# Performance work log

Measured on AMD Instinct MI355X. Metric: run time of the kernel, lower is better.

## Reference

```python
import jax, jax.numpy as jnp
import numpy as np

BETA = 0.25
N_CODES = 1024
CODE_DIM = 64


def setup_inputs() -> dict:
    key = jax.random.key(0)
    k1, k2 = jax.random.split(key)
    z_e = jax.random.normal(k1, (32, CODE_DIM, 2048), dtype=jnp.float32)
    # nn.init.uniform_(weight, -1/n_codes, 1/n_codes)
    lim = 1.0 / N_CODES
    codebook = jax.random.uniform(k2, (N_CODES, CODE_DIM), dtype=jnp.float32,
                                  minval=-lim, maxval=lim)
    return {"z_e": z_e, "codebook": codebook}


def reference(z_e, codebook):
    B, C, K = z_e.shape
    # (B, C, K) -> (B*K, C)
    z = jnp.transpose(z_e, (0, 2, 1)).reshape(-1, C)
    # squared L2 distances: ||z||^2 + ||e||^2 - 2 z.e  -> (N, n_codes)
    dist = (jnp.sum(z * z, axis=1, keepdims=True)
            + jnp.sum(codebook * codebook, axis=1)[None, :]
            - 2.0 * (z @ codebook.T))
    codes = jnp.argmin(dist, axis=1)  # (N,)
    # gather quantized vectors, back to (B, C, K)
    z_q = jnp.transpose(codebook[codes].reshape(B, K, C), (0, 2, 1))
    # straight-through
    z_q_st = z_e + jax.lax.stop_gradient(z_q - z_e)
    sg = jax.lax.stop_gradient
    loss_codebook = jnp.mean((z_q - sg(z_e)) ** 2)
    loss_commit = jnp.mean((z_e - sg(z_q)) ** 2)
    loss_vq = loss_codebook + BETA * loss_commit
    # perplexity via histogram (equivalent to onehot.mean(0))
    n = codes.shape[0]
    avg_probs = jnp.zeros((N_CODES,), dtype=jnp.float32).at[codes].add(1.0) / n
    perplexity = jnp.exp(-jnp.sum(avg_probs * jnp.log(avg_probs + 1e-10)))
    return z_q_st, codes.reshape(B, K), loss_vq, perplexity
```

## Files before the change

### kernel.cpp

```cpp
#include <hip/hip_runtime.h>
#include <math.h>

#define NB 32
#define NC 64
#define NK 2048
#define NCODES 1024
#define NVEC (NB*NK)
#define NELEM (NB*NC*NK)
#define NBLK (NVEC/64)

#define MARGIN 1.5e-3f
#define CAP 32

#define WS_HIST  0
#define WS_CBN32 4096
#define WS_PART  8192
#define WS_CTR   16384
#define WS_CBBF  32768

typedef __bf16 bf16x8 __attribute__((ext_vector_type(8)));
typedef float  f32x4  __attribute__((ext_vector_type(4)));
#define MFMA16(A, B, ACC) __builtin_amdgcn_mfma_f32_16x16x32_bf16(A, B, ACC, 0, 0, 0)

__global__ void k_cbprep(const float* __restrict__ cb, float* __restrict__ n32,
                         __bf16* __restrict__ cbbf, int* __restrict__ hist,
                         unsigned int* __restrict__ ctr) {
    const int t = threadIdx.x;
    const int j = blockIdx.x * 64 + t;
    if (blockIdx.x == 0) {
        int4 z4; z4.x = 0; z4.y = 0; z4.z = 0; z4.w = 0;
#pragma unroll
        for (int i = 0; i < 4; i++) ((int4*)hist)[t * 4 + i] = z4;
        if (t == 0) *ctr = 0u;
    }
    const float* cr = cb + (size_t)j * NC;
    float x[64];
#pragma unroll
    for (int i = 0; i < 16; i++) {
        f32x4 tv = *(const f32x4*)(cr + 4 * i);
        x[4*i+0] = tv[0]; x[4*i+1] = tv[1]; x[4*i+2] = tv[2]; x[4*i+3] = tv[3];
    }
    float r[8];
#pragma unroll
    for (int q = 0; q < 8; q++) r[q] = __fmul_rn(x[q], x[q]);
#pragma unroll
    for (int i = 8; i < 64; i += 8)
#pragma unroll
        for (int q = 0; q < 8; q++)
            r[q] = __fadd_rn(r[q], __fmul_rn(x[i + q], x[i + q]));
    float s01 = __fadd_rn(r[0], r[1]), s23 = __fadd_rn(r[2], r[3]);
    float s45 = __fadd_rn(r[4], r[5]), s67 = __fadd_rn(r[6], r[7]);
    n32[j] = __fadd_rn(__fadd_rn(s01, s23), __fadd_rn(s45, s67));
    __bf16* br = cbbf + (size_t)j * NC;
#pragma unroll
    for (int i = 0; i < 8; i++) {
        bf16x8 o;
#pragma unroll
        for (int q = 0; q < 8; q++) o[q] = (__bf16)x[8*i + q];
        *(bf16x8*)(br + 8*i) = o;
    }
}

__launch_bounds__(256, 4)
__global__ void k_vq(const float* __restrict__ ze, const float* __restrict__ cb,
                     const float* __restrict__ n32, const __bf16* __restrict__ cbbf,
                     int* __restrict__ hist, float* __restrict__ codes_f,
                     float* __restrict__ outq, double* __restrict__ part,
                     unsigned int* __restrict__ ctr, float* __restrict__ outsc) {
    __shared__ float zl[64 * 65];
    __shared__ float nl[NCODES];
    __shared__ float wmin[64][4];
    __shared__ float gthr[64];
    __shared__ int cnt[64];
    __shared__ int cand[64][CAP];
    __shared__ unsigned long long keys2[64][4];
    __shared__ int codearr[64];
    __shared__ double lsd[4];
    __shared__ int lastflag;
    __shared__ double TL[16], TE[16];

    const int t = threadIdx.x;
    const int L = t & 63;
    const int w = t >> 6;
    const int quad = L >> 4;
    const int col = L & 15;
    const int vec0 = blockIdx.x * 64;
    const int b = vec0 >> 11;
    const int k0 = vec0 & (NK - 1);
    const float* zbase = ze + (size_t)b * NC * NK + k0;

#pragma unroll
    for (int i = 0; i < 4; i++) {
        int idx = t + i * 256;
        int c = idx >> 4, vq = (idx & 15) * 4;
        f32x4 val = *(const f32x4*)(zbase + (size_t)c * NK + vq);
        zl[c * 65 + vq + 0] = val[0];
        zl[c * 65 + vq + 1] = val[1];
        zl[c * 65 + vq + 2] = val[2];
        zl[c * 65 + vq + 3] = val[3];
        nl[idx] = n32[idx];
    }
    __syncthreads();

    bf16x8 af[4][2];
#pragma unroll
    for (int vt = 0; vt < 4; vt++)
#pragma unroll
        for (int kt = 0; kt < 2; kt++)
#pragma unroll
            for (int j = 0; j < 8; j++)
                af[vt][kt][j] =
                    (__bf16)zl[(kt*32 + quad*8 + j) * 65 + vt*16 + col];

    float pmin[4][4];
#pragma unroll
    for (int vt = 0; vt < 4; vt++)
#pragma unroll
        for (int r = 0; r < 4; r++) pmin[vt][r] = 1e30f;
#pragma unroll 4
    for (int tile = 0; tile < 16; tile++) {
        const __bf16* brow = cbbf + (size_t)(w*256 + tile*16 + col) * NC + quad*8;
        bf16x8 b0 = *(const bf16x8*)(brow);
        bf16x8 b1 = *(const bf16x8*)(brow + 32);
        float nvv = nl[w*256 + tile*16 + col];
#pragma unroll
        for (int vt = 0; vt < 4; vt++) {
            f32x4 acc = {0.f, 0.f, 0.f, 0.f};
            acc = MFMA16(af[vt][0], b0, acc);
            acc = MFMA16(af[vt][1], b1, acc);
#pragma unroll
            for (int r = 0; r < 4; r++) {
                float pd = __fsub_rn(nvv, __fmul_rn(2.f, acc[r]));
                pmin[vt][r] = fminf(pmin[vt][r], pd);
            }
        }
    }
#pragma unroll
    for (int vt = 0; vt < 4; vt++)
#pragma unroll
        for (int r = 0; r < 4; r++) {
            float pm = pmin[vt][r];
            pm = fminf(pm, __shfl_xor(pm, 1, 16));
            pm = fminf(pm, __shfl_xor(pm, 2, 16));
            pm = fminf(pm, __shfl_xor(pm, 4, 16));
            pm = fminf(pm, __shfl_xor(pm, 8, 16));
            if (col == 0) wmin[vt*16 + quad*4 + r][w] = pm;
        }
    __syncthreads();

    if (t < 64) {
        float g = wmin[t][0];
#pragma unroll
        for (int ww = 1; ww < 4; ww++) g = fminf(g, wmin[t][ww]);
        gthr[t] = g + MARGIN;
        cnt[t] = 0;
    }
    __syncthreads();

    float thr[4][4];
#pragma unroll
    for (int vt = 0; vt < 4; vt++)
#pragma unroll
        for (int r = 0; r < 4; r++) thr[vt][r] = gthr[vt*16 + quad*4 + r];
#pragma unroll 4
    for (int tile = 0; tile < 16; tile++) {
        const __bf16* brow = cbbf + (size_t)(w*256 + tile*16 + col) * NC + quad*8;
        bf16x8 b0 = *(const bf16x8*)(brow);
        bf16x8 b1 = *(const bf16x8*)(brow + 32);
        float nvv = nl[w*256 + tile*16 + col];
#pragma unroll
        for (int vt = 0; vt < 4; vt++) {
            f32x4 acc = {0.f, 0.f, 0.f, 0.f};
            acc = MFMA16(af[vt][0], b0, acc);
            acc = MFMA16(af[vt][1], b1, acc);
#pragma unroll
            for (int r = 0; r < 4; r++) {
                float pd = __fsub_rn(nvv, __fmul_rn(2.f, acc[r]));
                if (pd <= thr[vt][r]) {
                    int m = vt*16 + quad*4 + r;
                    int slot = atomicAdd(&cnt[m], 1);
                    if (slot < CAP) cand[m][slot] = w*256 + tile*16 + col;
                }
            }
        }
    }
    __syncthreads();

    {
        const int v = L;
        float rr[8];
#pragma unroll
        for (int q = 0; q < 8; q++) {
            float xx = zl[q * 65 + v];
            rr[q] = __fmul_rn(xx, xx);
        }
#pragma unroll
        for (int i = 8; i < 64; i += 8)
#pragma unroll
            for (int q = 0; q < 8; q++) {
                float xx = zl[(i + q) * 65 + v];
                rr[q] = __fadd_rn(rr[q], __fmul_rn(xx, xx));
            }
        float s01 = __fadd_rn(rr[0], rr[1]), s23 = __fadd_rn(rr[2], rr[3]);
        float s45 = __fadd_rn(rr[4], rr[5]), s67 = __fadd_rn(rr[6], rr[7]);
        float t1 = __fadd_rn(__fadd_rn(s01, s23), __fadd_rn(s45, s67));

        int cc = cnt[v];
        unsigned long long kmin = 0xFFFFFFFFFFFFFFFFULL;
        if (cc <= CAP) {
            for (int si = w; si < cc; si += 4) {
                int j = cand[v][si];
                const float* cr = cb + (size_t)j * NC;
                float a = 0.f;
#pragma unroll
                for (int c = 0; c < NC; c++)
                    a = __fmaf_rn(zl[c * 65 + v], cr[c], a);
                float d = __fsub_rn(__fadd_rn(t1, nl[j]), __fmul_rn(2.f, a));
                unsigned long long key =
                    ((unsigned long long)__float_as_uint(d) << 32) | (unsigned int)j;
                if (key < kmin) kmin = key;
            }
        } else {
            for (int j = w * 256; j < (w + 1) * 256; j++) {
                const float* cr = cb + (size_t)j * NC;
                float a = 0.f;
#pragma unroll
                for (int c = 0; c < NC; c++)
                    a = __fmaf_rn(zl[c * 65 + v], cr[c], a);
                float d = __fsub_rn(__fadd_rn(t1, nl[j]), __fmul_rn(2.f, a));
                unsigned long long key =
                    ((unsigned long long)__float_as_uint(d) << 32) | (unsigned int)j;
                if (key < kmin) kmin = key;
            }
        }
        keys2[v][w] = kmin;
    }
    __syncthreads();

    if (t < 64) {
        unsigned long long kmin = keys2[t][0];
#pragma unroll
        for (int ww = 1; ww < 4; ww++) {
            unsigned long long kk = keys2[t][ww];
            if (kk < kmin) kmin = kk;
        }
        int code = (int)(kmin & 0xFFFFFFFFu);
        codearr[t] = code;
        codes_f[vec0 + t] = (float)code;
        atomicAdd(&hist[code], 1);
    }
    __syncthreads();

    double s = 0.0;
    float* ob = outq + (size_t)b * NC * NK + k0;
    const int c0 = t >> 4;
    const int v0 = (t & 15) * 4;
    int cds[4];
#pragma unroll
    for (int u = 0; u < 4; u++) cds[u] = codearr[v0 + u];
#pragma unroll
    for (int half = 0; half < 4; half++) {
        const int c = c0 + half * 16;
        f32x4 ov;
#pragma unroll
        for (int u = 0; u < 4; u++) {
            float zev = zl[c * 65 + v0 + u];
            float qv = cb[(size_t)cds[u] * NC + c];
            ov[u] = __fadd_rn(zev, __fsub_rn(qv, zev));
            double d = (double)qv - (double)zev;
            s += d * d;
        }
        *(f32x4*)(ob + (size_t)c * NK + v0) = ov;
    }
    for (int off = 32; off; off >>= 1) s += __shfl_down(s, off);
    if (L == 0) lsd[w] = s;
    __syncthreads();
    if (t == 0) {
        double tot = lsd[0] + lsd[1] + lsd[2] + lsd[3];
        part[blockIdx.x] = tot;
        __threadfence();
        unsigned int my = atomicAdd(ctr, 1u);
        lastflag = (my == NBLK - 1) ? 1 : 0;
    }
    __syncthreads();

    if (lastflag) {
        __threadfence();
#pragma unroll
        for (int gi = 0; gi < 4; gi++) {
            int g = w + gi * 4;
            double vL = part[g * 64 + L];
            double p = (double)hist[g * 64 + L] * (1.0 / (double)NVEC);
            double vE = p * log(p + 1e-10);
            for (int off = 32; off; off >>= 1) {
                vL += __shfl_down(vL, off);
                vE += __shfl_down(vE, off);
            }
            if (L == 0) { TL[g] = vL; TE[g] = vE; }
        }
        __syncthreads();
        if (t == 0) {
            double SL = 0.0, SE = 0.0;
#pragma unroll
            for (int i = 0; i < 16; i++) { SL += TL[i]; SE += TE[i]; }
            double loss_cb = SL / (double)NELEM;
            outsc[0] = (float)(loss_cb + 0.25 * loss_cb);
            outsc[1] = (float)exp(-SE);
        }
    }
}

extern "C" void kernel_launch(void* const* d_in, const int* in_sizes, int n_in,
                              void* d_out, int out_size, void* d_ws, size_t ws_size,
                              hipStream_t stream) {
    const float* ze = (const float*)d_in[0];
    const float* cb = (const float*)d_in[1];
    float* out = (float*)d_out;
    char* ws = (char*)d_ws;

    int*          hist = (int*)(ws + WS_HIST);
    float*        n32  = (float*)(ws + WS_CBN32);
    double*       part = (double*)(ws + WS_PART);
    unsigned int* ctr  = (unsigned int*)(ws + WS_CTR);
    __bf16*       cbbf = (__bf16*)(ws + WS_CBBF);

    float* zq      = out;
    float* codes_f = out + NELEM;
    float* outsc   = out + NELEM + NVEC;

    k_cbprep<<<16, 64, 0, stream>>>(cb, n32, cbbf, hist, ctr);
    k_vq<<<NBLK, 256, 0, stream>>>(ze, cb, n32, cbbf, hist, codes_f, zq, part,
                                   ctr, outsc);
}
```

Baseline: 151.9 us.

## Halve vectors per block, drop LDS staging, read z and norms from global

Each block now handles 32 vectors instead of 64, which doubles the grid to 2048 blocks and raises launch bounds to 8 waves per SIMD. The z tile and codebook-norm staging in shared memory is removed, so A-fragments, norms, the rescoring dot products and the output pass all read global memory (through cache) directly. Rescoring spreads candidates over 8 partitions per vector, and the final reduction handles 2048 partial sums. The aim is higher occupancy and less LDS use, but each codebook tile is now reused across only 32 vectors, so codebook and z traffic roughly doubles and uncoalesced strided global loads replace LDS reads.

```diff
diff --git a/kernel.cpp b/kernel.cpp
--- a/kernel.cpp
+++ b/kernel.cpp
@@ -7,7 +7,7 @@
 #define NCODES 1024
 #define NVEC (NB*NK)
 #define NELEM (NB*NC*NK)
-#define NBLK (NVEC/64)
+#define NBLK2 2048
 
 #define MARGIN 1.5e-3f
 #define CAP 32
@@ -15,7 +15,7 @@
 #define WS_HIST  0
 #define WS_CBN32 4096
 #define WS_PART  8192
-#define WS_CTR   16384
+#define WS_CTR   24576
 #define WS_CBBF  32768
 
 typedef __bf16 bf16x8 __attribute__((ext_vector_type(8)));
@@ -61,82 +61,67 @@
     }
 }
 
-__launch_bounds__(256, 4)
+__launch_bounds__(256, 8)
 __global__ void k_vq(const float* __restrict__ ze, const float* __restrict__ cb,
                      const float* __restrict__ n32, const __bf16* __restrict__ cbbf,
                      int* __restrict__ hist, float* __restrict__ codes_f,
                      float* __restrict__ outq, double* __restrict__ part,
                      unsigned int* __restrict__ ctr, float* __restrict__ outsc) {
-    __shared__ float zl[64 * 65];
-    __shared__ float nl[NCODES];
-    __shared__ float wmin[64][4];
-    __shared__ float gthr[64];
-    __shared__ int cnt[64];
-    __shared__ int cand[64][CAP];
-    __shared__ unsigned long long keys2[64][4];
-    __shared__ int codearr[64];
+    __shared__ float wmin[32][4];
+    __shared__ float gthr[32];
+    __shared__ int cnt[32];
+    __shared__ int cand[32][CAP];
+    __shared__ unsigned long long keys2[32][8];
+    __shared__ int codearr[32];
     __shared__ double lsd[4];
     __shared__ int lastflag;
-    __shared__ double TL[16], TE[16];
+    __shared__ double TL[32], TE[16];
 
     const int t = threadIdx.x;
     const int L = t & 63;
     const int w = t >> 6;
     const int quad = L >> 4;
     const int col = L & 15;
-    const int vec0 = blockIdx.x * 64;
+    const int vec0 = blockIdx.x * 32;
     const int b = vec0 >> 11;
     const int k0 = vec0 & (NK - 1);
     const float* zbase = ze + (size_t)b * NC * NK + k0;
 
-#pragma unroll
-    for (int i = 0; i < 4; i++) {
-        int idx = t + i * 256;
-        int c = idx >> 4, vq = (idx & 15) * 4;
-        f32x4 val = *(const f32x4*)(zbase + (size_t)c * NK + vq);
-        zl[c * 65 + vq + 0] = val[0];
-        zl[c * 65 + vq + 1] = val[1];
-        zl[c * 65 + vq + 2] = val[2];
-        zl[c * 65 + vq + 3] = val[3];
-        nl[idx] = n32[idx];
-    }
-    __syncthreads();
-
-    bf16x8 af[4][2];
-#pragma unroll
-    for (int vt = 0; vt < 4; vt++)
+    bf16x8 af[2][2];
+#pragma unroll
+    for (int vt = 0; vt < 2; vt++)
 #pragma unroll
         for (int kt = 0; kt < 2; kt++)
 #pragma unroll
             for (int j = 0; j < 8; j++)
                 af[vt][kt][j] =
-                    (__bf16)zl[(kt*32 + quad*8 + j) * 65 + vt*16 + col];
-
-    float pmin[4][4];
-#pragma unroll
-    for (int vt = 0; vt < 4; vt++)
+                    (__bf16)zbase[(size_t)(kt*32 + quad*8 + j) * NK + vt*16 + col];
+
+    float pmin[2][4];
+#pragma unroll
+    for (int vt = 0; vt < 2; vt++)
 #pragma unroll
         for (int r = 0; r < 4; r++) pmin[vt][r] = 1e30f;
-#pragma unroll 4
+#pragma unroll 2
     for (int tile = 0; tile < 16; tile++) {
         const __bf16* brow = cbbf + (size_t)(w*256 + tile*16 + col) * NC + quad*8;
         bf16x8 b0 = *(const bf16x8*)(brow);
         bf16x8 b1 = *(const bf16x8*)(brow + 32);
-        float nvv = nl[w*256 + tile*16 + col];
-#pragma unroll
-        for (int vt = 0; vt < 4; vt++) {
+        float nvv = n32[w*256 + tile*16 + col];
+#pragma unroll
+        for (int vt = 0; vt < 2; vt++) {
             f32x4 acc = {0.f, 0.f, 0.f, 0.f};
             acc = MFMA16(af[vt][0], b0, acc);
             acc = MFMA16(af[vt][1], b1, acc);
 #pragma unroll
             for (int r = 0; r < 4; r++) {
-                float pd = __fsub_rn(nvv, __fmul_rn(2.f, acc[r]));
+                float pd = __fmaf_rn(-2.f, acc[r], nvv);
                 pmin[vt][r] = fminf(pmin[vt][r], pd);
             }
         }
     }
 #pragma unroll
-    for (int vt = 0; vt < 4; vt++)
+    for (int vt = 0; vt < 2; vt++)
 #pragma unroll
         for (int r = 0; r < 4; r++) {
             float pm = pmin[vt][r];
@@ -148,7 +133,7 @@
         }
     __syncthreads();
 
-    if (t < 64) {
+    if (t < 32) {
         float g = wmin[t][0];
 #pragma unroll
         for (int ww = 1; ww < 4; ww++) g = fminf(g, wmin[t][ww]);
@@ -157,25 +142,25 @@
     }
     __syncthreads();
 
-    float thr[4][4];
-#pragma unroll
-    for (int vt = 0; vt < 4; vt++)
+    float thr[2][4];
+#pragma unroll
+    for (int vt = 0; vt < 2; vt++)
 #pragma unroll
         for (int r = 0; r < 4; r++) thr[vt][r] = gthr[vt*16 + quad*4 + r];
-#pragma unroll 4
+#pragma unroll 2
     for (int tile = 0; tile < 16; tile++) {
         const __bf16* brow = cbbf + (size_t)(w*256 + tile*16 + col) * NC + quad*8;
         bf16x8 b0 = *(const bf16x8*)(brow);
         bf16x8 b1 = *(const bf16x8*)(brow + 32);
-        float nvv = nl[w*256 + tile*16 + col];
-#pragma unroll
-        for (int vt = 0; vt < 4; vt++) {
+        float nvv = n32[w*256 + tile*16 + col];
+#pragma unroll
+        for (int vt = 0; vt < 2; vt++) {
             f32x4 acc = {0.f, 0.f, 0.f, 0.f};
             acc = MFMA16(af[vt][0], b0, acc);
             acc = MFMA16(af[vt][1], b1, acc);
 #pragma unroll
             for (int r = 0; r < 4; r++) {
-                float pd = __fsub_rn(nvv, __fmul_rn(2.f, acc[r]));
+                float pd = __fmaf_rn(-2.f, acc[r], nvv);
                 if (pd <= thr[vt][r]) {
                     int m = vt*16 + quad*4 + r;
                     int slot = atomicAdd(&cnt[m], 1);
@@ -187,18 +172,19 @@
     __syncthreads();
 
     {
-        const int v = L;
+        const int v = t & 31;
+        const int p = t >> 5;
         float rr[8];
 #pragma unroll
         for (int q = 0; q < 8; q++) {
-            float xx = zl[q * 65 + v];
+            float xx = zbase[(size_t)q * NK + v];
             rr[q] = __fmul_rn(xx, xx);
         }
 #pragma unroll
         for (int i = 8; i < 64; i += 8)
 #pragma unroll
             for (int q = 0; q < 8; q++) {
-                float xx = zl[(i + q) * 65 + v];
+                float xx = zbase[(size_t)(i + q) * NK + v];
                 rr[q] = __fadd_rn(rr[q], __fmul_rn(xx, xx));
             }
         float s01 = __fadd_rn(rr[0], rr[1]), s23 = __fadd_rn(rr[2], rr[3]);
@@ -208,40 +194,40 @@
         int cc = cnt[v];
         unsigned long long kmin = 0xFFFFFFFFFFFFFFFFULL;
         if (cc <= CAP) {
-            for (int si = w; si < cc; si += 4) {
+            for (int si = p; si < cc; si += 8) {
                 int j = cand[v][si];
                 const float* cr = cb + (size_t)j * NC;
                 float a = 0.f;
 #pragma unroll
                 for (int c = 0; c < NC; c++)
-                    a = __fmaf_rn(zl[c * 65 + v], cr[c], a);
-                float d = __fsub_rn(__fadd_rn(t1, nl[j]), __fmul_rn(2.f, a));
+                    a = __fmaf_rn(zbase[(size_t)c * NK + v], cr[c], a);
+                float d = __fmaf_rn(-2.f, a, __fadd_rn(t1, n32[j]));
                 unsigned long long key =
                     ((unsigned long long)__float_as_uint(d) << 32) | (unsigned int)j;
                 if (key < kmin) kmin = key;
             }
         } else {
-            for (int j = w * 256; j < (w + 1) * 256; j++) {
+            for (int j = p * 128; j < (p + 1) * 128; j++) {
                 const float* cr = cb + (size_t)j * NC;
                 float a = 0.f;
 #pragma unroll
                 for (int c = 0; c < NC; c++)
-                    a = __fmaf_rn(zl[c * 65 + v], cr[c], a);
-                float d = __fsub_rn(__fadd_rn(t1, nl[j]), __fmul_rn(2.f, a));
+                    a = __fmaf_rn(zbase[(size_t)c * NK + v], cr[c], a);
+                float d = __fmaf_rn(-2.f, a, __fadd_rn(t1, n32[j]));
                 unsigned long long key =
                     ((unsigned long long)__float_as_uint(d) << 32) | (unsigned int)j;
                 if (key < kmin) kmin = key;
             }
         }
-        keys2[v][w] = kmin;
-    }
-    __syncthreads();
-
-    if (t < 64) {
+        keys2[v][p] = kmin;
+    }
+    __syncthreads();
+
+    if (t < 32) {
         unsigned long long kmin = keys2[t][0];
 #pragma unroll
-        for (int ww = 1; ww < 4; ww++) {
-            unsigned long long kk = keys2[t][ww];
+        for (int pp = 1; pp < 8; pp++) {
+            unsigned long long kk = keys2[t][pp];
             if (kk < kmin) kmin = kk;
         }
         int code = (int)(kmin & 0xFFFFFFFFu);
@@ -253,21 +239,21 @@
 
     double s = 0.0;
     float* ob = outq + (size_t)b * NC * NK + k0;
-    const int c0 = t >> 4;
-    const int v0 = (t & 15) * 4;
+    const int c0 = t >> 3;
+    const int v0 = (t & 7) * 4;
     int cds[4];
 #pragma unroll
     for (int u = 0; u < 4; u++) cds[u] = codearr[v0 + u];
 #pragma unroll
-    for (int half = 0; half < 4; half++) {
-        const int c = c0 + half * 16;
+    for (int half = 0; half < 2; half++) {
+        const int c = c0 + half * 32;
+        f32x4 zv = *(const f32x4*)(zbase + (size_t)c * NK + v0);
         f32x4 ov;
 #pragma unroll
         for (int u = 0; u < 4; u++) {
-            float zev = zl[c * 65 + v0 + u];
             float qv = cb[(size_t)cds[u] * NC + c];
-            ov[u] = __fadd_rn(zev, __fsub_rn(qv, zev));
-            double d = (double)qv - (double)zev;
+            ov[u] = __fadd_rn(zv[u], __fsub_rn(qv, zv[u]));
+            double d = (double)qv - (double)zv[u];
             s += d * d;
         }
         *(f32x4*)(ob + (size_t)c * NK + v0) = ov;
@@ -280,29 +266,34 @@
         part[blockIdx.x] = tot;
         __threadfence();
         unsigned int my = atomicAdd(ctr, 1u);
-        lastflag = (my == NBLK - 1) ? 1 : 0;
+        lastflag = (my == NBLK2 - 1) ? 1 : 0;
     }
     __syncthreads();
 
     if (lastflag) {
         __threadfence();
 #pragma unroll
+        for (int gi = 0; gi < 8; gi++) {
+            int g = w + gi * 4;
+            double vL = part[g * 64 + L];
+            for (int off = 32; off; off >>= 1) vL += __shfl_down(vL, off);
+            if (L == 0) TL[g] = vL;
+        }
+#pragma unroll
         for (int gi = 0; gi < 4; gi++) {
             int g = w + gi * 4;
-            double vL = part[g * 64 + L];
-            double p = (double)hist[g * 64 + L] * (1.0 / (double)NVEC);
-            double vE = p * log(p + 1e-10);
-            for (int off = 32; off; off >>= 1) {
-                vL += __shfl_down(vL, off);
-                vE += __shfl_down(vE, off);
-            }
-            if (L == 0) { TL[g] = vL; TE[g] = vE; }
+            double pp = (double)hist[g * 64 + L] * (1.0 / (double)NVEC);
+            double vE = pp * log(pp + 1e-10);
+            for (int off = 32; off; off >>= 1) vE += __shfl_down(vE, off);
+            if (L == 0) TE[g] = vE;
         }
         __syncthreads();
         if (t == 0) {
             double SL = 0.0, SE = 0.0;
 #pragma unroll
-            for (int i = 0; i < 16; i++) { SL += TL[i]; SE += TE[i]; }
+            for (int i = 0; i < 32; i++) SL += TL[i];
+#pragma unroll
+            for (int i = 0; i < 16; i++) SE += TE[i];
             double loss_cb = SL / (double)NELEM;
             outsc[0] = (float)(loss_cb + 0.25 * loss_cb);
             outsc[1] = (float)exp(-SE);
@@ -329,6 +320,6 @@
     float* outsc   = out + NELEM + NVEC;
 
     k_cbprep<<<16, 64, 0, stream>>>(cb, n32, cbbf, hist, ctr);
-    k_vq<<<NBLK, 256, 0, stream>>>(ze, cb, n32, cbbf, hist, codes_f, zq, part,
-                                   ctr, outsc);
+    k_vq<<<NBLK2, 256, 0, stream>>>(ze, cb, n32, cbbf, hist, codes_f, zq, part,
+                                    ctr, outsc);
 }
```

After: 275.7 us. +81.5%, slower.
